# Kernel tuning notes

Measured on AMD Instinct MI355X. Metric: run time of the kernel, lower is better.

## Reference

```python
import jax, jax.numpy as jnp
import numpy as np

B, S, D, H = 2, 2048, 1024, 16
DH = D // H
LEVELS, FACTOR = 3, 2


def setup_inputs() -> dict:
    key = jax.random.key(0)
    ks = jax.random.split(key, 12)
    s = 1.0 / np.sqrt(D)
    n = lambda k, shape, sc: (jax.random.normal(k, shape, jnp.float32) * sc)
    return {
        "query": n(ks[0], (B, S, D), 1.0),
        "key": n(ks[1], (B, S, D), 1.0),
        "value": n(ks[2], (B, S, D), 1.0),
        "Wq": n(ks[3], (D, D), s), "bq": jnp.zeros((D,), jnp.float32),
        "Wk": n(ks[4], (D, D), s), "bk": jnp.zeros((D,), jnp.float32),
        "Wv": n(ks[5], (D, D), s), "bv": jnp.zeros((D,), jnp.float32),
        "Wo": n(ks[6], (D, D), s), "bo": jnp.zeros((D,), jnp.float32),
        "w_levels": jnp.ones((LEVELS,), jnp.float32),
    }


def _downsample(m):
    # mean-pool pairs along sequence: [B, S, D] -> [B, S//FACTOR, D]
    b, s, d = m.shape
    sn = s // FACTOR
    return m[:, : sn * FACTOR, :].reshape(b, sn, FACTOR, d).mean(axis=2)


def _mha(q, k, v, Wq, bq, Wk, bk, Wv, bv, Wo, bo):
    b, sq, d = q.shape
    sk = k.shape[1]
    qh = (q @ Wq + bq).reshape(b, sq, H, DH)
    kh = (k @ Wk + bk).reshape(b, sk, H, DH)
    vh = (v @ Wv + bv).reshape(b, sk, H, DH)
    scores = jnp.einsum("bqhd,bkhd->bhqk", qh, kh) / np.sqrt(DH)
    attn = jax.nn.softmax(scores, axis=-1)
    out = jnp.einsum("bhqk,bkhd->bqhd", attn, vh).reshape(b, sq, d)
    return out @ Wo + bo


def reference(query, key, value, Wq, bq, Wk, bk, Wv, bv, Wo, bo, w_levels):
    keys, vals = [key], [value]
    k_, v_ = key, value
    for _ in range(LEVELS - 1):
        k_ = _downsample(k_)
        v_ = _downsample(v_)
        keys.append(k_)
        vals.append(v_)
    acc = None
    for lvl in range(LEVELS):
        o = _mha(query, keys[lvl], vals[lvl], Wq, bq, Wk, bk, Wv, bv, Wo, bo)
        o = o * w_levels[lvl]
        acc = o if acc is None else acc + o
    return acc / w_levels.sum()
```

## Files before the change

kernel.cpp:

```cpp
#include <hip/hip_runtime.h>


#define B_  2
#define S_  2048
#define D_  1024
#define H_  16
#define DH_ 64
#define THR2 10.0f

typedef short s8v __attribute__((ext_vector_type(8)));
typedef float f4v __attribute__((ext_vector_type(4)));
typedef float f16v __attribute__((ext_vector_type(16)));
typedef unsigned int u32x2 __attribute__((ext_vector_type(2)));
typedef unsigned int u32x4 __attribute__((ext_vector_type(4)));

__device__ __forceinline__ unsigned cvtpk(float lo, float hi){
    unsigned r;
    asm volatile("v_cvt_pk_bf16_f32 %0, %1, %2" : "=v"(r) : "v"(lo), "v"(hi));
    return r;
}
__device__ __forceinline__ unsigned short f2bf1(float v){
    unsigned r;
    asm volatile("v_cvt_pk_bf16_f32 %0, %1, %2" : "=v"(r) : "v"(v), "v"(v));
    return (unsigned short)r;
}
__device__ __forceinline__ float bf2f(unsigned short h){
    union { unsigned u; float f; } v; v.u = ((unsigned)h) << 16;
    return v.f;
}
__device__ __forceinline__ float exp2_(float x){
    float r; asm("v_exp_f32 %0, %1" : "=v"(r) : "v"(x)); return r;
}
__device__ __forceinline__ void pswap(unsigned &dst, unsigned &src){
    asm volatile("v_permlane32_swap_b32 %0, %1" : "+v"(dst), "+v"(src));
}
__device__ __forceinline__ int swz(int row, int kb){
    return row*128 + (((kb) ^ (row & 7) ^ ((row >> 3) & 7)) << 4);
}

__global__ __launch_bounds__(256) void wtrans(
    const float* __restrict__ W0, const float* __restrict__ W1,
    const float* __restrict__ W2, const float* __restrict__ W3,
    unsigned short* __restrict__ T0, unsigned short* __restrict__ T1,
    unsigned short* __restrict__ T2, unsigned short* __restrict__ T3)
{
    __shared__ float tl[32][33];
    const float* W = blockIdx.z==0?W0: blockIdx.z==1?W1: blockIdx.z==2?W2:W3;
    unsigned short* T = blockIdx.z==0?T0: blockIdx.z==1?T1: blockIdx.z==2?T2:T3;
    const int t = threadIdx.x;
    const int bk = blockIdx.x*32, bn = blockIdx.y*32;
    {
        int row = t>>3, c4 = (t&7)*4;
        float4 v = *(const float4*)&W[(size_t)(bk+row)*D_ + bn + c4];
        tl[row][c4+0]=v.x; tl[row][c4+1]=v.y; tl[row][c4+2]=v.z; tl[row][c4+3]=v.w;
    }
    __syncthreads();
    {
        int n = t>>3, k4 = (t&7)*4;
        unsigned a = cvtpk(tl[k4+0][n], tl[k4+1][n]);
        unsigned b = cvtpk(tl[k4+2][n], tl[k4+3][n]);
        u32x2 pk = {a, b};
        *(u32x2*)&T[(size_t)(bn+n)*D_ + bk + k4] = pk;
    }
}

template<int MODE, int AF32>
__global__ __launch_bounds__(256) void gemm_mfma(
    const void* __restrict__ Av, const unsigned short* __restrict__ Btw,
    const float* __restrict__ bias, void* __restrict__ Cv, float scale)
{
    const int N_ = D_, K_ = D_;
    __shared__ __align__(16) char lds[65536];
    const int t = threadIdx.x;
    const int l = t & 63, wv = t>>6, g = l>>4, x = l&15;
    const int wr = wv>>1, wc = wv&1;
    const int br = blockIdx.y*128, bc = blockIdx.x*128;
    const float* Af = (const float*)Av;
    const unsigned short* Ab = (const unsigned short*)Av;

    int rw[4], bl[4];
    #pragma unroll
    for (int p=0;p<4;++p){ int u = t + 256*p; rw[p] = u>>3; bl[p] = u&7; }

    f4v acc[4][4];
    #pragma unroll
    for (int i=0;i<4;++i)
        #pragma unroll
        for (int j=0;j<4;++j) acc[i][j] = (f4v){0.f,0.f,0.f,0.f};

    float4 alo[4], ahi[4]; s8v arg[4]; s8v brg[4];
    #pragma unroll
    for (int p=0;p<4;++p){
        if (AF32){
            const float* ap = Af + (size_t)(br+rw[p])*K_ + bl[p]*8;
            alo[p] = *(const float4*)ap; ahi[p] = *(const float4*)(ap+4);
        } else {
            arg[p] = *(const s8v*)(Ab + (size_t)(br+rw[p])*K_ + bl[p]*8);
        }
        brg[p] = *(const s8v*)(Btw + (size_t)(bc+rw[p])*K_ + bl[p]*8);
    }

    int cur = 0;
    for (int kt=0; kt<K_; kt+=64){
        char* AsB = lds + cur*32768;
        char* BsB = AsB + 16384;
        #pragma unroll
        for (int p=0;p<4;++p){
            if (AF32){
                uint4 pk;
                pk.x = cvtpk(alo[p].x, alo[p].y); pk.y = cvtpk(alo[p].z, alo[p].w);
                pk.z = cvtpk(ahi[p].x, ahi[p].y); pk.w = cvtpk(ahi[p].z, ahi[p].w);
                *(uint4*)(AsB + swz(rw[p], bl[p])) = pk;
            } else {
                *(s8v*)(AsB + swz(rw[p], bl[p])) = arg[p];
            }
            *(s8v*)(BsB + swz(rw[p], bl[p])) = brg[p];
        }
        if (kt + 64 < K_){
            #pragma unroll
            for (int p=0;p<4;++p){
                if (AF32){
                    const float* ap = Af + (size_t)(br+rw[p])*K_ + (kt+64) + bl[p]*8;
                    alo[p] = *(const float4*)ap; ahi[p] = *(const float4*)(ap+4);
                } else {
                    arg[p] = *(const s8v*)(Ab + (size_t)(br+rw[p])*K_ + (kt+64) + bl[p]*8);
                }
                brg[p] = *(const s8v*)(Btw + (size_t)(bc+rw[p])*K_ + (kt+64) + bl[p]*8);
            }
        }
        __syncthreads();
        #pragma unroll
        for (int c=0;c<2;++c){
            s8v af[4], bf[4];
            #pragma unroll
            for (int fm=0; fm<4; ++fm)
                af[fm] = *(const s8v*)(AsB + swz(wr*64+fm*16+x, c*4+g));
            #pragma unroll
            for (int fn=0; fn<4; ++fn)
                bf[fn] = *(const s8v*)(BsB + swz(wc*64+fn*16+x, c*4+g));
            __builtin_amdgcn_s_setprio(1);
            #pragma unroll
            for (int fm=0; fm<4; ++fm)
                #pragma unroll
                for (int fn=0; fn<4; ++fn)
                    acc[fm][fn] = __builtin_amdgcn_mfma_f32_16x16x32_bf16(
                        af[fm], bf[fn], acc[fm][fn], 0,0,0);
            __builtin_amdgcn_s_setprio(0);
        }
        cur ^= 1;
    }

    #pragma unroll
    for (int fn=0; fn<4; ++fn){
        int col = bc + wc*64 + fn*16 + x;
        float bv = bias[col];
        #pragma unroll
        for (int fm=0; fm<4; ++fm){
            int row0 = br + wr*64 + fm*16 + g*4;
            float v0 = (acc[fm][fn][0] + bv);
            float v1 = (acc[fm][fn][1] + bv);
            float v2 = (acc[fm][fn][2] + bv);
            float v3 = (acc[fm][fn][3] + bv);
            if (MODE == 0){
                float* C = (float*)Cv;
                C[(size_t)(row0+0)*N_ + col] = v0;
                C[(size_t)(row0+1)*N_ + col] = v1;
                C[(size_t)(row0+2)*N_ + col] = v2;
                C[(size_t)(row0+3)*N_ + col] = v3;
            } else if (MODE == 1){
                unsigned short* C = (unsigned short*)Cv;
                int hI = col>>6, dhI = col & (DH_-1);
                #pragma unroll
                for (int r=0;r<4;++r){
                    int row = row0 + r;
                    int bI = row>>11, sI = row & (S_-1);
                    float vv = (r==0?v0: r==1?v1: r==2?v2: v3) * scale;
                    C[(((size_t)(bI*H_+hI))*S_+sI)*DH_+dhI] = f2bf1(vv);
                }
            } else {
                unsigned short* C = (unsigned short*)Cv;
                int bI = row0>>11, sI = row0 & (S_-1);
                int hI = col>>6, dhI = col & (DH_-1);
                u32x2 pk;
                pk.x = cvtpk(v0*scale, v1*scale);
                pk.y = cvtpk(v2*scale, v3*scale);
                *(u32x2*)&C[(((size_t)(bI*H_+hI))*DH_+dhI)*S_ + sI] = pk;
            }
        }
    }
}

__global__ __launch_bounds__(256) void pool2_bf16(
    const unsigned short* __restrict__ in, unsigned short* __restrict__ out,
    int nOut4, int Sin)
{
    int idx = blockIdx.x * 256 + threadIdx.x;
    if (idx >= nOut4) return;
    int d0   = (idx & 15) * 4;
    int rest = idx >> 4;
    int Sout = Sin >> 1;
    int so = rest % Sout;
    int bh = rest / Sout;
    size_t base = ((size_t)bh * Sin + 2*so) * DH_ + d0;
    ushort4 a = *(const ushort4*)&in[base];
    ushort4 c = *(const ushort4*)&in[base + DH_];
    ushort4 o;
    o.x = f2bf1(0.5f*(bf2f(a.x)+bf2f(c.x)));
    o.y = f2bf1(0.5f*(bf2f(a.y)+bf2f(c.y)));
    o.z = f2bf1(0.5f*(bf2f(a.z)+bf2f(c.z)));
    o.w = f2bf1(0.5f*(bf2f(a.w)+bf2f(c.w)));
    *(ushort4*)&out[(size_t)idx*4] = o;
}

__global__ __launch_bounds__(256) void pool2T(
    const unsigned short* __restrict__ in, unsigned short* __restrict__ out,
    int nOut4, int Sin, int shift)
{
    int idx = blockIdx.x * 256 + threadIdx.x;
    if (idx >= nOut4) return;
    int row = idx >> shift;
    int so4 = (idx & ((1<<shift)-1)) << 2;
    union { u32x4 u; unsigned short h[8]; } a;
    a.u = *(const u32x4*)&in[(size_t)row*Sin + so4*2];
    float m0 = 0.5f*(bf2f(a.h[0])+bf2f(a.h[1]));
    float m1 = 0.5f*(bf2f(a.h[2])+bf2f(a.h[3]));
    float m2 = 0.5f*(bf2f(a.h[4])+bf2f(a.h[5]));
    float m3 = 0.5f*(bf2f(a.h[6])+bf2f(a.h[7]));
    u32x2 pk; pk.x = cvtpk(m0,m1); pk.y = cvtpk(m2,m3);
    *(u32x2*)&out[(size_t)row*(Sin>>1) + so4] = pk;
}

__global__ __launch_bounds__(256, 2) void attn_mfma5(
    const unsigned short* __restrict__ qh,
    const unsigned short* __restrict__ kh0, const unsigned short* __restrict__ kh1,
    const unsigned short* __restrict__ kh2,
    const unsigned short* __restrict__ vt0, const unsigned short* __restrict__ vt1,
    const unsigned short* __restrict__ vt2,
    const float* __restrict__ wlv, unsigned short* __restrict__ accOut)
{
    __shared__ __align__(16) char ksm[2][8192];
    __shared__ __align__(16) char vsm[2][8192];
    const int t = threadIdx.x, l = t&63, wv = t>>6, q = l&31, hi = l>>5;
    const int bid = blockIdx.x;
    const int qt = bid & 15, h = (bid>>4) & (H_-1), b = bid >> 8;

    const float w0 = wlv[0], w1 = wlv[1], w2 = wlv[2];
    const float winv = 1.f/(w0+w1+w2);

    const unsigned short* qp =
        qh + (((size_t)(b*H_+h))*S_ + (size_t)qt*128 + wv*32 + q)*DH_ + hi*8;
    s8v qf0 = *(const s8v*)(qp);
    s8v qf1 = *(const s8v*)(qp + 16);
    s8v qf2 = *(const s8v*)(qp + 32);
    s8v qf3 = *(const s8v*)(qp + 48);

    const int r0 = t>>3, kb = t&7;
    const int off0 = swz(r0, kb), off1 = swz(r0+32, kb);

    f16v aO0, aO1;
    #pragma unroll
    for (int r=0;r<16;++r){ aO0[r]=0.f; aO1[r]=0.f; }

    int cur = 0;
    #pragma unroll 1
    for (int lvl = 0; lvl < 3; ++lvl) {
        const unsigned short *kp, *vpt; int nt; float wc;
        if (lvl == 0)      { kp = kh0; vpt = vt0; nt = 32; wc = w0; }
        else if (lvl == 1) { kp = kh1; vpt = vt1; nt = 16; wc = w1; }
        else               { kp = kh2; vpt = vt2; nt = 8;  wc = w2; }
        const int Sl = nt*64;
        const unsigned short* kbase = kp + (size_t)(b*H_+h)*Sl*DH_;
        const unsigned short* v0r = vpt + ((size_t)(b*H_+h)*DH_ + r0)*Sl;
        const unsigned short* v1r = vpt + ((size_t)(b*H_+h)*DH_ + r0+32)*Sl;

        float m_i = -1e30f, l_i = 0.f;
        f16v o0, o1;
        #pragma unroll
        for (int r=0;r<16;++r){ o0[r]=0.f; o1[r]=0.f; }

        s8v krg0 = *(const s8v*)(kbase + (size_t)r0*DH_ + kb*8);
        s8v krg1 = *(const s8v*)(kbase + (size_t)(r0+32)*DH_ + kb*8);
        s8v vrg0 = *(const s8v*)(v0r + kb*8);
        s8v vrg1 = *(const s8v*)(v1r + kb*8);

        for (int kt = 0; kt < nt; ++kt) {
            char* kb_ = ksm[cur];
            char* vb_ = vsm[cur];
            *(s8v*)(kb_ + off0) = krg0;
            *(s8v*)(kb_ + off1) = krg1;
            *(s8v*)(vb_ + off0) = vrg0;
            *(s8v*)(vb_ + off1) = vrg1;
            if (kt + 1 < nt) {
                size_t nb = (size_t)(kt+1)*64;
                krg0 = *(const s8v*)(kbase + (nb+r0)*DH_ + kb*8);
                krg1 = *(const s8v*)(kbase + (nb+r0+32)*DH_ + kb*8);
                vrg0 = *(const s8v*)(v0r + nb + kb*8);
                vrg1 = *(const s8v*)(v1r + nb + kb*8);
            }
            __syncthreads();

            f16v s0, s1;
            #pragma unroll
            for (int r=0;r<16;++r){ s0[r]=0.f; s1[r]=0.f; }
            {
                s8v k00 = *(const s8v*)(kb_ + swz(q,      0*2+hi));
                s8v k01 = *(const s8v*)(kb_ + swz(q,      1*2+hi));
                s8v k02 = *(const s8v*)(kb_ + swz(q,      2*2+hi));
                s8v k03 = *(const s8v*)(kb_ + swz(q,      3*2+hi));
                s8v k10 = *(const s8v*)(kb_ + swz(32+q,   0*2+hi));
                s8v k11 = *(const s8v*)(kb_ + swz(32+q,   1*2+hi));
                s8v k12 = *(const s8v*)(kb_ + swz(32+q,   2*2+hi));
                s8v k13 = *(const s8v*)(kb_ + swz(32+q,   3*2+hi));
                __builtin_amdgcn_s_setprio(1);
                s0 = __builtin_amdgcn_mfma_f32_32x32x16_bf16(k00, qf0, s0, 0,0,0);
                s1 = __builtin_amdgcn_mfma_f32_32x32x16_bf16(k10, qf0, s1, 0,0,0);
                s0 = __builtin_amdgcn_mfma_f32_32x32x16_bf16(k01, qf1, s0, 0,0,0);
                s1 = __builtin_amdgcn_mfma_f32_32x32x16_bf16(k11, qf1, s1, 0,0,0);
                s0 = __builtin_amdgcn_mfma_f32_32x32x16_bf16(k02, qf2, s0, 0,0,0);
                s1 = __builtin_amdgcn_mfma_f32_32x32x16_bf16(k12, qf2, s1, 0,0,0);
                s0 = __builtin_amdgcn_mfma_f32_32x32x16_bf16(k03, qf3, s0, 0,0,0);
                s1 = __builtin_amdgcn_mfma_f32_32x32x16_bf16(k13, qf3, s1, 0,0,0);
                __builtin_amdgcn_s_setprio(0);
            }

            float pm = s0[0];
            #pragma unroll
            for (int r=1;r<16;++r) pm = fmaxf(pm, s0[r]);
            #pragma unroll
            for (int r=0;r<16;++r) pm = fmaxf(pm, s1[r]);
            pm = fmaxf(pm, __shfl_xor(pm, 32, 64));
            if (__any(pm > m_i + THR2)) {
                float mn = fmaxf(m_i, pm);
                float corr = exp2_(m_i - mn);
                m_i = mn;
                l_i *= corr;
                #pragma unroll
                for (int r=0;r<16;++r){
                    float cb = __shfl(corr, ((r&3)+8*(r>>2)) + 4*hi, 64);
                    o0[r] *= cb; o1[r] *= cb;
                }
            }
            float rs = 0.f;
            #pragma unroll
            for (int r=0;r<16;++r){ s0[r] = exp2_(s0[r]-m_i); rs += s0[r]; }
            #pragma unroll
            for (int r=0;r<16;++r){ s1[r] = exp2_(s1[r]-m_i); rs += s1[r]; }
            rs += __shfl_xor(rs, 32, 64);
            l_i += rs;

            unsigned a0 = cvtpk(s0[0], s0[1]),  a1 = cvtpk(s0[2], s0[3]);
            unsigned b0 = cvtpk(s0[4], s0[5]),  b1 = cvtpk(s0[6], s0[7]);
            pswap(a0, b0); pswap(a1, b1);
            unsigned c0 = cvtpk(s0[8], s0[9]),  c1 = cvtpk(s0[10], s0[11]);
            unsigned d0 = cvtpk(s0[12], s0[13]),d1 = cvtpk(s0[14], s0[15]);
            pswap(c0, d0); pswap(c1, d1);
            unsigned e0 = cvtpk(s1[0], s1[1]),  e1 = cvtpk(s1[2], s1[3]);
            unsigned f0 = cvtpk(s1[4], s1[5]),  f1 = cvtpk(s1[6], s1[7]);
            pswap(e0, f0); pswap(e1, f1);
            unsigned g0 = cvtpk(s1[8], s1[9]),  g1 = cvtpk(s1[10], s1[11]);
            unsigned h0 = cvtpk(s1[12], s1[13]),h1 = cvtpk(s1[14], s1[15]);
            pswap(g0, h0); pswap(g1, h1);
            union { u32x4 u; s8v s; } pf0, pf1, pf2, pf3;
            pf0.u = (u32x4){a0, a1, b0, b1};
            pf1.u = (u32x4){c0, c1, d0, d1};
            pf2.u = (u32x4){e0, e1, f0, f1};
            pf3.u = (u32x4){g0, g1, h0, h1};

            {
                s8v v00 = *(const s8v*)(vb_ + swz(q,    0*2+hi));
                s8v v01 = *(const s8v*)(vb_ + swz(q,    1*2+hi));
                s8v v02 = *(const s8v*)(vb_ + swz(q,    2*2+hi));
                s8v v03 = *(const s8v*)(vb_ + swz(q,    3*2+hi));
                s8v v10 = *(const s8v*)(vb_ + swz(32+q, 0*2+hi));
                s8v v11 = *(const s8v*)(vb_ + swz(32+q, 1*2+hi));
                s8v v12 = *(const s8v*)(vb_ + swz(32+q, 2*2+hi));
                s8v v13 = *(const s8v*)(vb_ + swz(32+q, 3*2+hi));
                __builtin_amdgcn_s_setprio(1);
                o0 = __builtin_amdgcn_mfma_f32_32x32x16_bf16(pf0.s, v00, o0, 0,0,0);
                o1 = __builtin_amdgcn_mfma_f32_32x32x16_bf16(pf0.s, v10, o1, 0,0,0);
                o0 = __builtin_amdgcn_mfma_f32_32x32x16_bf16(pf1.s, v01, o0, 0,0,0);
                o1 = __builtin_amdgcn_mfma_f32_32x32x16_bf16(pf1.s, v11, o1, 0,0,0);
                o0 = __builtin_amdgcn_mfma_f32_32x32x16_bf16(pf2.s, v02, o0, 0,0,0);
                o1 = __builtin_amdgcn_mfma_f32_32x32x16_bf16(pf2.s, v12, o1, 0,0,0);
                o0 = __builtin_amdgcn_mfma_f32_32x32x16_bf16(pf3.s, v03, o0, 0,0,0);
                o1 = __builtin_amdgcn_mfma_f32_32x32x16_bf16(pf3.s, v13, o1, 0,0,0);
                __builtin_amdgcn_s_setprio(0);
            }
            cur ^= 1;
        }

        float wl = wc * winv;
        #pragma unroll
        for (int r=0;r<16;++r){
            float lb = __shfl(l_i, ((r&3)+8*(r>>2)) + 4*hi, 64);
            float sc = wl / lb;
            aO0[r] += o0[r] * sc;
            aO1[r] += o1[r] * sc;
        }
    }

    #pragma unroll
    for (int r=0;r<16;++r){
        int qrow = ((r&3)+8*(r>>2)) + 4*hi;
        size_t row = (size_t)b*S_ + (size_t)qt*128 + wv*32 + qrow;
        accOut[row*D_ + h*DH_ + q]      = f2bf1(aO0[r]);
        accOut[row*D_ + h*DH_ + 32 + q] = f2bf1(aO1[r]);
    }
}

extern "C" void kernel_launch(void* const* d_in, const int* in_sizes, int n_in,
                              void* d_out, int out_size, void* d_ws, size_t ws_size,
                              hipStream_t stream)
{
    const float* query = (const float*)d_in[0];
    const float* key   = (const float*)d_in[1];
    const float* value = (const float*)d_in[2];
    const float* Wq = (const float*)d_in[3];  const float* bq = (const float*)d_in[4];
    const float* Wk = (const float*)d_in[5];  const float* bk = (const float*)d_in[6];
    const float* Wv = (const float*)d_in[7];  const float* bv = (const float*)d_in[8];
    const float* Wo = (const float*)d_in[9];  const float* bo = (const float*)d_in[10];
    const float* wlv = (const float*)d_in[11];

    char* w = (char*)d_ws;
    unsigned short* qhb  = (unsigned short*)(w);
    unsigned short* khb0 = (unsigned short*)(w + 8388608);
    unsigned short* khb1 = (unsigned short*)(w + 16777216);
    unsigned short* khb2 = (unsigned short*)(w + 20971520);
    unsigned short* vtb0 = (unsigned short*)(w + 23068672);
    unsigned short* vtb1 = (unsigned short*)(w + 31457280);
    unsigned short* vtb2 = (unsigned short*)(w + 35651584);
    unsigned short* accb = (unsigned short*)(w + 37748736);
    unsigned short* Wtq  = (unsigned short*)(w + 46137344);
    unsigned short* Wtk  = (unsigned short*)(w + 48234496);
    unsigned short* Wtv  = (unsigned short*)(w + 50331648);
    unsigned short* Wto  = (unsigned short*)(w + 52428800);

    dim3 bb(256);
    wtrans<<<dim3(32,32,4), bb, 0, stream>>>(Wq, Wk, Wv, Wo, Wtq, Wtk, Wtv, Wto);

    const float scale_q = 0.125f * 1.44269504088896f;
    dim3 gg(D_/128, (B_*S_)/128);
    gemm_mfma<1,1><<<gg, bb, 0, stream>>>(query, Wtq, bq, qhb,  scale_q);
    gemm_mfma<1,1><<<gg, bb, 0, stream>>>(key,   Wtk, bk, khb0, 1.0f);
    gemm_mfma<2,1><<<gg, bb, 0, stream>>>(value, Wtv, bv, vtb0, 1.0f);

    int n1 = B_ * H_ * (S_/2) * DH_ / 4;
    int n2 = B_ * H_ * (S_/4) * DH_ / 4;
    pool2_bf16<<<n1/256, bb, 0, stream>>>(khb0, khb1, n1, S_);
    pool2_bf16<<<n2/256, bb, 0, stream>>>(khb1, khb2, n2, S_/2);
    pool2T<<<n1/256, bb, 0, stream>>>(vtb0, vtb1, n1, S_,   8);
    pool2T<<<n2/256, bb, 0, stream>>>(vtb1, vtb2, n2, S_/2, 7);

    attn_mfma5<<<B_*H_*(S_/128), bb, 0, stream>>>(qhb, khb0, khb1, khb2,
                                                  vtb0, vtb1, vtb2, wlv, accb);

    gemm_mfma<0,0><<<gg, bb, 0, stream>>>(accb, Wto, bo, d_out, 1.0f);
}
```

Baseline: 189.5 us.

## Batch QKV GEMMs, merge pool launches, split-KV attention with direct LDS loads

The three QKV projection GEMMs become one launch indexed by blockIdx.z. They now use a single LDS buffer with two barriers, so more blocks fit per CU. The output GEMM uses 64-row tiles so more blocks cover the GPU, and the K and V pooling kernels are merged into paired launches. Attention now runs 512-thread blocks: two groups of waves each process half the KV tiles, loaded with global_load_lds, and their online-softmax partials are merged through LDS at each level. This adds barriers and a combine step in exchange for more parallelism and fewer launches.

```diff
diff --git a/kernel.cpp b/kernel.cpp
--- a/kernel.cpp
+++ b/kernel.cpp
@@ -36,6 +36,11 @@
 }
 __device__ __forceinline__ int swz(int row, int kb){
     return row*128 + (((kb) ^ (row & 7) ^ ((row >> 3) & 7)) << 4);
+}
+__device__ __forceinline__ void gld16(const void* g, void* l){
+    __builtin_amdgcn_global_load_lds(
+        (const __attribute__((address_space(1))) unsigned int*)g,
+        (__attribute__((address_space(3))) unsigned int*)l, 16, 0, 0);
 }
 
 __global__ __launch_bounds__(256) void wtrans(
@@ -64,19 +69,29 @@
     }
 }
 
-template<int MODE, int AF32>
-__global__ __launch_bounds__(256) void gemm_mfma(
-    const void* __restrict__ Av, const unsigned short* __restrict__ Btw,
-    const float* __restrict__ bias, void* __restrict__ Cv, float scale)
+__global__ __launch_bounds__(256, 3) void gemm_qkv(
+    const float* __restrict__ Aq, const float* __restrict__ Ak, const float* __restrict__ Avv,
+    const unsigned short* __restrict__ Wq_, const unsigned short* __restrict__ Wk_,
+    const unsigned short* __restrict__ Wv_,
+    const float* __restrict__ bq_, const float* __restrict__ bk_, const float* __restrict__ bv_,
+    unsigned short* __restrict__ Oq, unsigned short* __restrict__ Ok,
+    unsigned short* __restrict__ Ov, float scale_q)
 {
+    const int z = blockIdx.z;
+    const float* A = z==0?Aq : z==1?Ak : Avv;
+    const unsigned short* Btw = z==0?Wq_ : z==1?Wk_ : Wv_;
+    const float* bias = z==0?bq_ : z==1?bk_ : bv_;
+    unsigned short* C = z==0?Oq : z==1?Ok : Ov;
+    const float scale = z==0? scale_q : 1.0f;
+    const int mode = (z==2) ? 2 : 1;
+
     const int N_ = D_, K_ = D_;
-    __shared__ __align__(16) char lds[65536];
+    __shared__ __align__(16) char lds[32768];
+    char* AsB = lds; char* BsB = lds + 16384;
     const int t = threadIdx.x;
     const int l = t & 63, wv = t>>6, g = l>>4, x = l&15;
     const int wr = wv>>1, wc = wv&1;
     const int br = blockIdx.y*128, bc = blockIdx.x*128;
-    const float* Af = (const float*)Av;
-    const unsigned short* Ab = (const unsigned short*)Av;
 
     int rw[4], bl[4];
     #pragma unroll
@@ -88,47 +103,33 @@
         #pragma unroll
         for (int j=0;j<4;++j) acc[i][j] = (f4v){0.f,0.f,0.f,0.f};
 
-    float4 alo[4], ahi[4]; s8v arg[4]; s8v brg[4];
+    float4 alo[4], ahi[4]; s8v brg[4];
     #pragma unroll
     for (int p=0;p<4;++p){
-        if (AF32){
-            const float* ap = Af + (size_t)(br+rw[p])*K_ + bl[p]*8;
-            alo[p] = *(const float4*)ap; ahi[p] = *(const float4*)(ap+4);
-        } else {
-            arg[p] = *(const s8v*)(Ab + (size_t)(br+rw[p])*K_ + bl[p]*8);
-        }
+        const float* ap = A + (size_t)(br+rw[p])*K_ + bl[p]*8;
+        alo[p] = *(const float4*)ap; ahi[p] = *(const float4*)(ap+4);
         brg[p] = *(const s8v*)(Btw + (size_t)(bc+rw[p])*K_ + bl[p]*8);
     }
 
-    int cur = 0;
     for (int kt=0; kt<K_; kt+=64){
-        char* AsB = lds + cur*32768;
-        char* BsB = AsB + 16384;
+        __syncthreads();
         #pragma unroll
         for (int p=0;p<4;++p){
-            if (AF32){
-                uint4 pk;
-                pk.x = cvtpk(alo[p].x, alo[p].y); pk.y = cvtpk(alo[p].z, alo[p].w);
-                pk.z = cvtpk(ahi[p].x, ahi[p].y); pk.w = cvtpk(ahi[p].z, ahi[p].w);
-                *(uint4*)(AsB + swz(rw[p], bl[p])) = pk;
-            } else {
-                *(s8v*)(AsB + swz(rw[p], bl[p])) = arg[p];
-            }
+            uint4 pk;
+            pk.x = cvtpk(alo[p].x, alo[p].y); pk.y = cvtpk(alo[p].z, alo[p].w);
+            pk.z = cvtpk(ahi[p].x, ahi[p].y); pk.w = cvtpk(ahi[p].z, ahi[p].w);
+            *(uint4*)(AsB + swz(rw[p], bl[p])) = pk;
             *(s8v*)(BsB + swz(rw[p], bl[p])) = brg[p];
         }
+        __syncthreads();
         if (kt + 64 < K_){
             #pragma unroll
             for (int p=0;p<4;++p){
-                if (AF32){
-                    const float* ap = Af + (size_t)(br+rw[p])*K_ + (kt+64) + bl[p]*8;
-                    alo[p] = *(const float4*)ap; ahi[p] = *(const float4*)(ap+4);
-                } else {
-                    arg[p] = *(const s8v*)(Ab + (size_t)(br+rw[p])*K_ + (kt+64) + bl[p]*8);
-                }
+                const float* ap = A + (size_t)(br+rw[p])*K_ + (kt+64) + bl[p]*8;
+                alo[p] = *(const float4*)ap; ahi[p] = *(const float4*)(ap+4);
                 brg[p] = *(const s8v*)(Btw + (size_t)(bc+rw[p])*K_ + (kt+64) + bl[p]*8);
             }
         }
-        __syncthreads();
         #pragma unroll
         for (int c=0;c<2;++c){
             s8v af[4], bf[4];
@@ -147,7 +148,6 @@
                         af[fm], bf[fn], acc[fm][fn], 0,0,0);
             __builtin_amdgcn_s_setprio(0);
         }
-        cur ^= 1;
     }
 
     #pragma unroll
@@ -157,18 +157,11 @@
         #pragma unroll
         for (int fm=0; fm<4; ++fm){
             int row0 = br + wr*64 + fm*16 + g*4;
-            float v0 = (acc[fm][fn][0] + bv);
-            float v1 = (acc[fm][fn][1] + bv);
-            float v2 = (acc[fm][fn][2] + bv);
-            float v3 = (acc[fm][fn][3] + bv);
-            if (MODE == 0){
-                float* C = (float*)Cv;
-                C[(size_t)(row0+0)*N_ + col] = v0;
-                C[(size_t)(row0+1)*N_ + col] = v1;
-                C[(size_t)(row0+2)*N_ + col] = v2;
-                C[(size_t)(row0+3)*N_ + col] = v3;
-            } else if (MODE == 1){
-                unsigned short* C = (unsigned short*)Cv;
+            float v0 = acc[fm][fn][0] + bv;
+            float v1 = acc[fm][fn][1] + bv;
+            float v2 = acc[fm][fn][2] + bv;
+            float v3 = acc[fm][fn][3] + bv;
+            if (mode == 1){
                 int hI = col>>6, dhI = col & (DH_-1);
                 #pragma unroll
                 for (int r=0;r<4;++r){
@@ -178,7 +171,6 @@
                     C[(((size_t)(bI*H_+hI))*S_+sI)*DH_+dhI] = f2bf1(vv);
                 }
             } else {
-                unsigned short* C = (unsigned short*)Cv;
                 int bI = row0>>11, sI = row0 & (S_-1);
                 int hI = col>>6, dhI = col & (DH_-1);
                 u32x2 pk;
@@ -190,47 +182,119 @@
     }
 }
 
-__global__ __launch_bounds__(256) void pool2_bf16(
-    const unsigned short* __restrict__ in, unsigned short* __restrict__ out,
-    int nOut4, int Sin)
+__global__ __launch_bounds__(256, 2) void gemm_out(
+    const unsigned short* __restrict__ Ab, const unsigned short* __restrict__ Btw,
+    const float* __restrict__ bias, float* __restrict__ C)
 {
-    int idx = blockIdx.x * 256 + threadIdx.x;
-    if (idx >= nOut4) return;
-    int d0   = (idx & 15) * 4;
-    int rest = idx >> 4;
-    int Sout = Sin >> 1;
-    int so = rest % Sout;
-    int bh = rest / Sout;
-    size_t base = ((size_t)bh * Sin + 2*so) * DH_ + d0;
-    ushort4 a = *(const ushort4*)&in[base];
-    ushort4 c = *(const ushort4*)&in[base + DH_];
-    ushort4 o;
-    o.x = f2bf1(0.5f*(bf2f(a.x)+bf2f(c.x)));
-    o.y = f2bf1(0.5f*(bf2f(a.y)+bf2f(c.y)));
-    o.z = f2bf1(0.5f*(bf2f(a.z)+bf2f(c.z)));
-    o.w = f2bf1(0.5f*(bf2f(a.w)+bf2f(c.w)));
-    *(ushort4*)&out[(size_t)idx*4] = o;
-}
-
-__global__ __launch_bounds__(256) void pool2T(
-    const unsigned short* __restrict__ in, unsigned short* __restrict__ out,
+    const int N_ = D_, K_ = D_;
+    __shared__ __align__(16) char lds[24576];
+    char* AsB = lds;
+    char* BsB = lds + 8192;
+    const int t = threadIdx.x, l = t&63, wv = t>>6, g = l>>4, x = l&15;
+    const int br = blockIdx.y*64, bc = blockIdx.x*128;
+
+    int arw[2], abl[2];
+    #pragma unroll
+    for (int p=0;p<2;++p){ int u = t + 256*p; arw[p] = u>>3; abl[p] = u&7; }
+    int brw[4], bbl[4];
+    #pragma unroll
+    for (int p=0;p<4;++p){ int u = t + 256*p; brw[p] = u>>3; bbl[p] = u&7; }
+
+    f4v acc[4][2];
+    #pragma unroll
+    for (int i=0;i<4;++i){ acc[i][0] = (f4v){0,0,0,0}; acc[i][1] = (f4v){0,0,0,0}; }
+
+    s8v arg[2], brg[4];
+    #pragma unroll
+    for (int p=0;p<2;++p) arg[p] = *(const s8v*)(Ab + (size_t)(br+arw[p])*K_ + abl[p]*8);
+    #pragma unroll
+    for (int p=0;p<4;++p) brg[p] = *(const s8v*)(Btw + (size_t)(bc+brw[p])*K_ + bbl[p]*8);
+
+    for (int kt=0; kt<K_; kt+=64){
+        __syncthreads();
+        #pragma unroll
+        for (int p=0;p<2;++p) *(s8v*)(AsB + swz(arw[p], abl[p])) = arg[p];
+        #pragma unroll
+        for (int p=0;p<4;++p) *(s8v*)(BsB + swz(brw[p], bbl[p])) = brg[p];
+        __syncthreads();
+        if (kt + 64 < K_){
+            #pragma unroll
+            for (int p=0;p<2;++p)
+                arg[p] = *(const s8v*)(Ab + (size_t)(br+arw[p])*K_ + (kt+64) + abl[p]*8);
+            #pragma unroll
+            for (int p=0;p<4;++p)
+                brg[p] = *(const s8v*)(Btw + (size_t)(bc+brw[p])*K_ + (kt+64) + bbl[p]*8);
+        }
+        #pragma unroll
+        for (int c=0;c<2;++c){
+            s8v af[4], bf[2];
+            #pragma unroll
+            for (int fm=0; fm<4; ++fm)
+                af[fm] = *(const s8v*)(AsB + swz(fm*16+x, c*4+g));
+            #pragma unroll
+            for (int fn=0; fn<2; ++fn)
+                bf[fn] = *(const s8v*)(BsB + swz(wv*32+fn*16+x, c*4+g));
+            __builtin_amdgcn_s_setprio(1);
+            #pragma unroll
+            for (int fm=0; fm<4; ++fm)
+                #pragma unroll
+                for (int fn=0; fn<2; ++fn)
+                    acc[fm][fn] = __builtin_amdgcn_mfma_f32_16x16x32_bf16(
+                        af[fm], bf[fn], acc[fm][fn], 0,0,0);
+            __builtin_amdgcn_s_setprio(0);
+        }
+    }
+
+    #pragma unroll
+    for (int fn=0; fn<2; ++fn){
+        int col = bc + wv*32 + fn*16 + x;
+        float bv = bias[col];
+        #pragma unroll
+        for (int fm=0; fm<4; ++fm){
+            int row0 = br + fm*16 + g*4;
+            #pragma unroll
+            for (int r=0;r<4;++r)
+                C[(size_t)(row0+r)*N_ + col] = acc[fm][fn][r] + bv;
+        }
+    }
+}
+
+__global__ __launch_bounds__(256) void pool_pair(
+    const unsigned short* __restrict__ kin, unsigned short* __restrict__ kout,
+    const unsigned short* __restrict__ vin, unsigned short* __restrict__ vout,
     int nOut4, int Sin, int shift)
 {
     int idx = blockIdx.x * 256 + threadIdx.x;
     if (idx >= nOut4) return;
-    int row = idx >> shift;
-    int so4 = (idx & ((1<<shift)-1)) << 2;
-    union { u32x4 u; unsigned short h[8]; } a;
-    a.u = *(const u32x4*)&in[(size_t)row*Sin + so4*2];
-    float m0 = 0.5f*(bf2f(a.h[0])+bf2f(a.h[1]));
-    float m1 = 0.5f*(bf2f(a.h[2])+bf2f(a.h[3]));
-    float m2 = 0.5f*(bf2f(a.h[4])+bf2f(a.h[5]));
-    float m3 = 0.5f*(bf2f(a.h[6])+bf2f(a.h[7]));
-    u32x2 pk; pk.x = cvtpk(m0,m1); pk.y = cvtpk(m2,m3);
-    *(u32x2*)&out[(size_t)row*(Sin>>1) + so4] = pk;
-}
-
-__global__ __launch_bounds__(256, 2) void attn_mfma5(
+    if (blockIdx.z == 0){
+        int d0 = (idx & 15) * 4;
+        int rest = idx >> 4;
+        int Sout = Sin >> 1;
+        int so = rest % Sout, bh = rest / Sout;
+        size_t base = ((size_t)bh * Sin + 2*so) * DH_ + d0;
+        ushort4 a = *(const ushort4*)&kin[base];
+        ushort4 c = *(const ushort4*)&kin[base + DH_];
+        ushort4 o;
+        o.x = f2bf1(0.5f*(bf2f(a.x)+bf2f(c.x)));
+        o.y = f2bf1(0.5f*(bf2f(a.y)+bf2f(c.y)));
+        o.z = f2bf1(0.5f*(bf2f(a.z)+bf2f(c.z)));
+        o.w = f2bf1(0.5f*(bf2f(a.w)+bf2f(c.w)));
+        *(ushort4*)&kout[(size_t)idx*4] = o;
+    } else {
+        int row = idx >> shift;
+        int so4 = (idx & ((1<<shift)-1)) << 2;
+        union { u32x4 u; unsigned short hh[8]; } a;
+        a.u = *(const u32x4*)&vin[(size_t)row*Sin + so4*2];
+        float m0 = 0.5f*(bf2f(a.hh[0])+bf2f(a.hh[1]));
+        float m1 = 0.5f*(bf2f(a.hh[2])+bf2f(a.hh[3]));
+        float m2 = 0.5f*(bf2f(a.hh[4])+bf2f(a.hh[5]));
+        float m3 = 0.5f*(bf2f(a.hh[6])+bf2f(a.hh[7]));
+        u32x2 pk; pk.x = cvtpk(m0,m1); pk.y = cvtpk(m2,m3);
+        *(u32x2*)&vout[(size_t)row*(Sin>>1) + so4] = pk;
+    }
+}
+
+__global__ __launch_bounds__(512, 4) void attn_mfma6(
     const unsigned short* __restrict__ qh,
     const unsigned short* __restrict__ kh0, const unsigned short* __restrict__ kh1,
     const unsigned short* __restrict__ kh2,
@@ -238,66 +302,80 @@
     const unsigned short* __restrict__ vt2,
     const float* __restrict__ wlv, unsigned short* __restrict__ accOut)
 {
-    __shared__ __align__(16) char ksm[2][8192];
-    __shared__ __align__(16) char vsm[2][8192];
-    const int t = threadIdx.x, l = t&63, wv = t>>6, q = l&31, hi = l>>5;
+    __shared__ __align__(16) char lds[65536];
+    const int t = threadIdx.x, l = t&63, wv = t>>6;
+    const int q = l&31, hi = l>>5;
+    const int half = wv>>2, wq = wv&3;
     const int bid = blockIdx.x;
-    const int qt = bid & 15, h = (bid>>4) & (H_-1), b = bid >> 8;
-
-    const float w0 = wlv[0], w1 = wlv[1], w2 = wlv[2];
+    const int qt = bid & 15, h = (bid>>4)&(H_-1), b = bid>>8;
+
+    const float w0=wlv[0], w1=wlv[1], w2=wlv[2];
     const float winv = 1.f/(w0+w1+w2);
 
     const unsigned short* qp =
-        qh + (((size_t)(b*H_+h))*S_ + (size_t)qt*128 + wv*32 + q)*DH_ + hi*8;
+        qh + (((size_t)(b*H_+h))*S_ + (size_t)qt*128 + wq*32 + q)*DH_ + hi*8;
     s8v qf0 = *(const s8v*)(qp);
-    s8v qf1 = *(const s8v*)(qp + 16);
-    s8v qf2 = *(const s8v*)(qp + 32);
-    s8v qf3 = *(const s8v*)(qp + 48);
-
-    const int r0 = t>>3, kb = t&7;
-    const int off0 = swz(r0, kb), off1 = swz(r0+32, kb);
-
-    f16v aO0, aO1;
-    #pragma unroll
-    for (int r=0;r<16;++r){ aO0[r]=0.f; aO1[r]=0.f; }
+    s8v qf1 = *(const s8v*)(qp+16);
+    s8v qf2 = *(const s8v*)(qp+32);
+    s8v qf3 = *(const s8v*)(qp+48);
+
+    const int lr = l>>3, lc = l&7;
+    const int isV = (wq>>1)&1;
+    const int wbase = (wq&1)*32, wb8 = (wq&1)*4;
+    int chs[4];
+    #pragma unroll
+    for (int j=0;j<4;++j) chs[j] = lc ^ lr ^ ((wb8 + j)&7);
+    int koff[4];
+    #pragma unroll
+    for (int j=0;j<4;++j) koff[j] = ((wbase + j*8 + lr)*DH_ + chs[j]*8)*2;
+
+    f16v accO0, accO1;
+    #pragma unroll
+    for (int r=0;r<16;++r){ accO0[r]=0.f; accO1[r]=0.f; }
 
     int cur = 0;
     #pragma unroll 1
-    for (int lvl = 0; lvl < 3; ++lvl) {
-        const unsigned short *kp, *vpt; int nt; float wc;
-        if (lvl == 0)      { kp = kh0; vpt = vt0; nt = 32; wc = w0; }
-        else if (lvl == 1) { kp = kh1; vpt = vt1; nt = 16; wc = w1; }
-        else               { kp = kh2; vpt = vt2; nt = 8;  wc = w2; }
+    for (int lvl=0; lvl<3; ++lvl){
+        const unsigned short *kp, *vp; int nt; float wgt;
+        if (lvl==0)      { kp = kh0; vp = vt0; nt = 32; wgt = w0; }
+        else if (lvl==1) { kp = kh1; vp = vt1; nt = 16; wgt = w1; }
+        else             { kp = kh2; vp = vt2; nt = 8;  wgt = w2; }
         const int Sl = nt*64;
-        const unsigned short* kbase = kp + (size_t)(b*H_+h)*Sl*DH_;
-        const unsigned short* v0r = vpt + ((size_t)(b*H_+h)*DH_ + r0)*Sl;
-        const unsigned short* v1r = vpt + ((size_t)(b*H_+h)*DH_ + r0+32)*Sl;
+        const char* gK = (const char*)(kp + (size_t)(b*H_+h)*Sl*DH_);
+        const char* gV = (const char*)(vp + (size_t)(b*H_+h)*DH_*Sl);
+        int voff[4];
+        #pragma unroll
+        for (int j=0;j<4;++j) voff[j] = ((wbase + j*8 + lr)*Sl + chs[j]*8)*2;
 
         float m_i = -1e30f, l_i = 0.f;
         f16v o0, o1;
         #pragma unroll
         for (int r=0;r<16;++r){ o0[r]=0.f; o1[r]=0.f; }
 
-        s8v krg0 = *(const s8v*)(kbase + (size_t)r0*DH_ + kb*8);
-        s8v krg1 = *(const s8v*)(kbase + (size_t)(r0+32)*DH_ + kb*8);
-        s8v vrg0 = *(const s8v*)(v0r + kb*8);
-        s8v vrg1 = *(const s8v*)(v1r + kb*8);
-
-        for (int kt = 0; kt < nt; ++kt) {
-            char* kb_ = ksm[cur];
-            char* vb_ = vsm[cur];
-            *(s8v*)(kb_ + off0) = krg0;
-            *(s8v*)(kb_ + off1) = krg1;
-            *(s8v*)(vb_ + off0) = vrg0;
-            *(s8v*)(vb_ + off1) = vrg1;
-            if (kt + 1 < nt) {
-                size_t nb = (size_t)(kt+1)*64;
-                krg0 = *(const s8v*)(kbase + (nb+r0)*DH_ + kb*8);
-                krg1 = *(const s8v*)(kbase + (nb+r0+32)*DH_ + kb*8);
-                vrg0 = *(const s8v*)(v0r + nb + kb*8);
-                vrg1 = *(const s8v*)(v1r + nb + kb*8);
-            }
+        const int nt2 = nt>>1;
+        {
+            char* lb0 = lds + cur*32768 + half*16384 + isV*8192;
+            const char* g0 = isV ? (gV + half*128) : (gK + half*8192);
+            const int* off = isV ? voff : koff;
+            #pragma unroll
+            for (int j=0;j<4;++j)
+                gld16(g0 + off[j], lb0 + (wbase + j*8)*128);
+        }
+        #pragma unroll 1
+        for (int rd=0; rd<nt2; ++rd){
+            asm volatile("s_waitcnt vmcnt(0)" ::: "memory");
             __syncthreads();
+            if (rd+1 < nt2){
+                int tile = 2*(rd+1) + half;
+                char* lb1 = lds + (cur^1)*32768 + half*16384 + isV*8192;
+                const char* g1 = isV ? (gV + tile*128) : (gK + tile*8192);
+                const int* off = isV ? voff : koff;
+                #pragma unroll
+                for (int j=0;j<4;++j)
+                    gld16(g1 + off[j], lb1 + (wbase + j*8)*128);
+            }
+            char* kb_ = lds + cur*32768 + half*16384;
+            char* vb_ = kb_ + 8192;
 
             f16v s0, s1;
             #pragma unroll
@@ -323,11 +401,19 @@
                 __builtin_amdgcn_s_setprio(0);
             }
 
-            float pm = s0[0];
-            #pragma unroll
-            for (int r=1;r<16;++r) pm = fmaxf(pm, s0[r]);
-            #pragma unroll
-            for (int r=0;r<16;++r) pm = fmaxf(pm, s1[r]);
+            float pm;
+            {
+                float a0 = fmaxf(fmaxf(s0[0],s0[1]),   fmaxf(s0[2],s0[3]));
+                float a1 = fmaxf(fmaxf(s0[4],s0[5]),   fmaxf(s0[6],s0[7]));
+                float a2 = fmaxf(fmaxf(s0[8],s0[9]),   fmaxf(s0[10],s0[11]));
+                float a3 = fmaxf(fmaxf(s0[12],s0[13]), fmaxf(s0[14],s0[15]));
+                float a4 = fmaxf(fmaxf(s1[0],s1[1]),   fmaxf(s1[2],s1[3]));
+                float a5 = fmaxf(fmaxf(s1[4],s1[5]),   fmaxf(s1[6],s1[7]));
+                float a6 = fmaxf(fmaxf(s1[8],s1[9]),   fmaxf(s1[10],s1[11]));
+                float a7 = fmaxf(fmaxf(s1[12],s1[13]), fmaxf(s1[14],s1[15]));
+                pm = fmaxf(fmaxf(fmaxf(a0,a1),fmaxf(a2,a3)),
+                           fmaxf(fmaxf(a4,a5),fmaxf(a6,a7)));
+            }
             pm = fmaxf(pm, __shfl_xor(pm, 32, 64));
             if (__any(pm > m_i + THR2)) {
                 float mn = fmaxf(m_i, pm);
@@ -389,22 +475,59 @@
             cur ^= 1;
         }
 
-        float wl = wc * winv;
+        float wl = wgt * winv;
+        __syncthreads();
+        if (half == 1){
+            char* scr = lds;
+            #pragma unroll
+            for (int g4=0; g4<4; ++g4){
+                float4 a; a.x=o0[g4*4+0]; a.y=o0[g4*4+1]; a.z=o0[g4*4+2]; a.w=o0[g4*4+3];
+                *(float4*)(scr + wq*4096 + g4*1024 + l*16) = a;
+                float4 c; c.x=o1[g4*4+0]; c.y=o1[g4*4+1]; c.z=o1[g4*4+2]; c.w=o1[g4*4+3];
+                *(float4*)(scr + 16384 + wq*4096 + g4*1024 + l*16) = c;
+            }
+            *(float*)(lds + 32768 + wq*256 + l*4) = m_i;
+            *(float*)(lds + 33792 + wq*256 + l*4) = l_i;
+        }
+        __syncthreads();
+        if (half == 0){
+            char* scr = lds;
+            float mp = *(const float*)(lds + 32768 + wq*256 + l*4);
+            float lp = *(const float*)(lds + 33792 + wq*256 + l*4);
+            float mm  = fmaxf(m_i, mp);
+            float ca  = exp2_(m_i - mm);
+            float cb2 = exp2_(mp  - mm);
+            float lm  = l_i*ca + lp*cb2;
+            float po0[16], po1[16];
+            #pragma unroll
+            for (int g4=0; g4<4; ++g4){
+                float4 a = *(const float4*)(scr + wq*4096 + g4*1024 + l*16);
+                po0[g4*4+0]=a.x; po0[g4*4+1]=a.y; po0[g4*4+2]=a.z; po0[g4*4+3]=a.w;
+                float4 c = *(const float4*)(scr + 16384 + wq*4096 + g4*1024 + l*16);
+                po1[g4*4+0]=c.x; po1[g4*4+1]=c.y; po1[g4*4+2]=c.z; po1[g4*4+3]=c.w;
+            }
+            #pragma unroll
+            for (int r=0;r<16;++r){
+                int qr = ((r&3)+8*(r>>2)) + 4*hi;
+                float caB = __shfl(ca,  qr, 64);
+                float cbB = __shfl(cb2, qr, 64);
+                float lB  = __shfl(lm,  qr, 64);
+                float sc = wl / lB;
+                accO0[r] += (o0[r]*caB + po0[r]*cbB) * sc;
+                accO1[r] += (o1[r]*caB + po1[r]*cbB) * sc;
+            }
+        }
+        __syncthreads();
+    }
+
+    if (half == 0){
         #pragma unroll
         for (int r=0;r<16;++r){
-            float lb = __shfl(l_i, ((r&3)+8*(r>>2)) + 4*hi, 64);
-            float sc = wl / lb;
-            aO0[r] += o0[r] * sc;
-            aO1[r] += o1[r] * sc;
-        }
-    }
-
-    #pragma unroll
-    for (int r=0;r<16;++r){
-        int qrow = ((r&3)+8*(r>>2)) + 4*hi;
-        size_t row = (size_t)b*S_ + (size_t)qt*128 + wv*32 + qrow;
-        accOut[row*D_ + h*DH_ + q]      = f2bf1(aO0[r]);
-        accOut[row*D_ + h*DH_ + 32 + q] = f2bf1(aO1[r]);
+            int qrow = ((r&3)+8*(r>>2)) + 4*hi;
+            size_t row = (size_t)b*S_ + (size_t)qt*128 + wq*32 + qrow;
+            accOut[row*D_ + h*DH_ + q]      = f2bf1(accO0[r]);
+            accOut[row*D_ + h*DH_ + 32 + q] = f2bf1(accO1[r]);
+        }
     }
 }
 
@@ -439,20 +562,17 @@
     wtrans<<<dim3(32,32,4), bb, 0, stream>>>(Wq, Wk, Wv, Wo, Wtq, Wtk, Wtv, Wto);
 
     const float scale_q = 0.125f * 1.44269504088896f;
-    dim3 gg(D_/128, (B_*S_)/128);
-    gemm_mfma<1,1><<<gg, bb, 0, stream>>>(query, Wtq, bq, qhb,  scale_q);
-    gemm_mfma<1,1><<<gg, bb, 0, stream>>>(key,   Wtk, bk, khb0, 1.0f);
-    gemm_mfma<2,1><<<gg, bb, 0, stream>>>(value, Wtv, bv, vtb0, 1.0f);
+    gemm_qkv<<<dim3(8,32,3), bb, 0, stream>>>(query, key, value,
+                                              Wtq, Wtk, Wtv, bq, bk, bv,
+                                              qhb, khb0, vtb0, scale_q);
 
     int n1 = B_ * H_ * (S_/2) * DH_ / 4;
     int n2 = B_ * H_ * (S_/4) * DH_ / 4;
-    pool2_bf16<<<n1/256, bb, 0, stream>>>(khb0, khb1, n1, S_);
-    pool2_bf16<<<n2/256, bb, 0, stream>>>(khb1, khb2, n2, S_/2);
-    pool2T<<<n1/256, bb, 0, stream>>>(vtb0, vtb1, n1, S_,   8);
-    pool2T<<<n2/256, bb, 0, stream>>>(vtb1, vtb2, n2, S_/2, 7);
-
-    attn_mfma5<<<B_*H_*(S_/128), bb, 0, stream>>>(qhb, khb0, khb1, khb2,
-                                                  vtb0, vtb1, vtb2, wlv, accb);
-
-    gemm_mfma<0,0><<<gg, bb, 0, stream>>>(accb, Wto, bo, d_out, 1.0f);
-}
+    pool_pair<<<dim3(n1/256,1,2), bb, 0, stream>>>(khb0, khb1, vtb0, vtb1, n1, S_,   8);
+    pool_pair<<<dim3(n2/256,1,2), bb, 0, stream>>>(khb1, khb2, vtb1, vtb2, n2, S_/2, 7);
+
+    attn_mfma6<<<512, 512, 0, stream>>>(qhb, khb0, khb1, khb2,
+                                        vtb0, vtb1, vtb2, wlv, accb);
+
+    gemm_out<<<dim3(8,64), bb, 0, stream>>>(accb, Wto, bo, (float*)d_out);
+}
```

Measured after the change: 327.2 us. +72.6%, slower.
